# Kernel tuning notes

Measured on AMD Instinct MI355X. Metric: run time of the kernel, lower is better.

## Reference

```python
import jax, jax.numpy as jnp
import numpy as np

N_NODES = 100000


def _gcn_conv(x, W, b, row, col, norm, n):
    # PyG GCNConv: h = x @ W, then symmetric-normalized scatter-add, then bias
    h = x @ W                          # [N, out]
    msg = h[col] * norm[:, None]       # gather at source nodes, scale per-edge
    out = jax.ops.segment_sum(msg, row, num_segments=n)  # scatter-add to dest
    return out + b


def setup_inputs() -> dict:
    key = jax.random.key(0)
    k1, k2, k3, k4, k5, k6 = jax.random.split(key, 6)
    F_in, H, C = 128, 128, 64
    E = 1600000
    x = jax.random.normal(k1, (N_NODES, F_in), dtype=jnp.float32)
    edge_index = jax.random.randint(k2, (2, E), 0, N_NODES, dtype=jnp.int64)
    s1 = 1.0 / np.sqrt(F_in)
    s2 = 1.0 / np.sqrt(H)
    W1 = jax.random.uniform(k3, (F_in, H), jnp.float32, -s1, s1)
    b1 = jax.random.uniform(k4, (H,), jnp.float32, -s1, s1)
    W2 = jax.random.uniform(k5, (H, C), jnp.float32, -s2, s2)
    b2 = jax.random.uniform(k6, (C,), jnp.float32, -s2, s2)
    return {"x": x, "edge_index": edge_index, "W1": W1, "b1": b1, "W2": W2, "b2": b2}


def reference(x, edge_index, W1, b1, W2, b2):
    n = x.shape[0]
    # add self-loops (GCNConv default)
    loops = jnp.arange(n, dtype=edge_index.dtype)
    row = jnp.concatenate([edge_index[0], loops])  # destination
    col = jnp.concatenate([edge_index[1], loops])  # source
    # symmetric normalization deg^{-1/2}[row] * deg^{-1/2}[col]
    deg = jax.ops.segment_sum(jnp.ones_like(row, dtype=x.dtype), row, num_segments=n)
    dinv = jnp.where(deg > 0, jax.lax.rsqrt(deg), 0.0)
    norm = dinv[row] * dinv[col]       # [E+N]
    h = jax.nn.relu(_gcn_conv(x, W1, b1, row, col, norm, n))
    # dropout is identity in eval mode
    out = _gcn_conv(h, W2, b2, row, col, norm, n)
    return jax.nn.log_softmax(out, axis=1)
```

## Files before the change

kernel.cpp:

```cpp
#include <hip/hip_runtime.h>
#include <hip/hip_fp16.h>
#include <cstdint>
#include <cstddef>

#define TPB 256
#define CAP 64
#define FWSHIFT 9
#define FWROWS 512
#define CAPB 96
#define DEC_ITERS 32


using half8 = __attribute__((ext_vector_type(8))) _Float16;
using f32x4 = __attribute__((ext_vector_type(4))) float;

struct GemmSm {
    _Float16 Wl[32 * 64 * 8];
    _Float16 Of[4][16 * 136];
};
struct DecSm { int cur[256]; int bad; };
union SetupSm { GemmSm g; DecSm d; };

__global__ __launch_bounds__(256)
void k_setup(const void* __restrict__ ei, int E, int N,
             const float* __restrict__ W1, const float* __restrict__ W2,
             _Float16* __restrict__ wf2,
             int2* __restrict__ bpairs, int* __restrict__ bcnt,
             int nDec, int nFW,
             const float* __restrict__ x, __half* __restrict__ xw1, int nGemm) {
    __shared__ __align__(16) SetupSm sm;
    const int b = blockIdx.x;
    const int tid = threadIdx.x;

    if (b < 8) {
        int i = b * TPB + tid;
        int k  = i >> 4;
        int n0 = (i & 15) * 4;
        float4 w = ((const float4*)W2)[i];
        int ct = n0 >> 4, kb = k >> 5;
        int lane0 = ((k >> 3) & 3) * 16 + (n0 & 15);
        int j = k & 7;
        int base = ((ct * 4 + kb) * 64 + lane0) * 8 + j;
        wf2[base]      = (_Float16)w.x;
        wf2[base + 8]  = (_Float16)w.y;
        wf2[base + 16] = (_Float16)w.z;
        wf2[base + 24] = (_Float16)w.w;
    } else if (b < 8 + nDec) {
        const int dblk = b - 8;
        if (tid == 0) sm.d.bad = 0;
        for (int f = tid; f < nFW; f += TPB) sm.d.cur[f] = 0;
        __syncthreads();
        {
            long long v = ((const long long*)ei)[tid];
            if (v < 0 || v >= (long long)N) sm.d.bad = 1;
        }
        __syncthreads();
        const int is64 = !sm.d.bad;
        const int base = dblk * (TPB * DEC_ITERS);
        const long long* e64 = (const long long*)ei;
        const int* e32 = (const int*)ei;

        for (int it = 0; it < DEC_ITERS; it += 4) {
            int d[4], s[4]; bool val[4];
#pragma unroll
            for (int k = 0; k < 4; ++k) {
                int e = base + (it + k) * TPB + tid;
                val[k] = e < E;
                if (val[k]) {
                    if (is64) { d[k] = (int)e64[e]; s[k] = (int)e64[(long long)E + e]; }
                    else      { d[k] = e32[e];      s[k] = e32[E + e]; }
                }
            }
#pragma unroll
            for (int k = 0; k < 4; ++k) {
                if (val[k]) {
                    int fw  = d[k] >> FWSHIFT;
                    int pos = atomicAdd(&sm.d.cur[fw], 1);
                    if (pos < CAPB)
                        bpairs[((size_t)fw * nDec + dblk) * CAPB + pos] =
                            make_int2(d[k], s[k]);
                }
            }
        }
        __syncthreads();
        for (int f = tid; f < nFW; f += TPB) {
            int c = sm.d.cur[f];
            bcnt[(size_t)f * nDec + dblk] = c > CAPB ? CAPB : c;
        }
    } else {
        const int gb = b - 8 - nDec;
        for (int i = tid; i < 4096; i += TPB) {
            float4 w = ((const float4*)W1)[i];
            int k  = i >> 5;
            int n0 = (i & 31) * 4;
            int ct = n0 >> 4, kb = k >> 5;
            int lane0 = ((k >> 3) & 3) * 16 + (n0 & 15);
            int j = k & 7;
            int bs = ((ct * 4 + kb) * 64 + lane0) * 8 + j;
            sm.g.Wl[bs]      = (_Float16)w.x;
            sm.g.Wl[bs + 8]  = (_Float16)w.y;
            sm.g.Wl[bs + 16] = (_Float16)w.z;
            sm.g.Wl[bs + 24] = (_Float16)w.w;
        }
        __syncthreads();
        const half8* wl = (const half8*)sm.g.Wl;
        const int wave = tid >> 6, lane = tid & 63;
        const int m = lane & 15, quad = lane >> 4;
        const int nRowTiles = (N + 15) >> 4;

        for (int rt = gb * 4 + wave; rt < nRowTiles; rt += nGemm * 4) {
            const int row0 = rt * 16;
            const int arow = row0 + m;
            const bool rvalid = arow < N;
            const float* xrow = x + (size_t)(rvalid ? arow : 0) * 128;

            f32x4 acc[8];
#pragma unroll
            for (int ct = 0; ct < 8; ++ct) acc[ct] = (f32x4){0.f, 0.f, 0.f, 0.f};

#pragma unroll
            for (int kb = 0; kb < 4; ++kb) {
                const float4* ap = (const float4*)(xrow + kb * 32 + quad * 8);
                float4 a0 = ap[0], a1 = ap[1];
                half8 a;
                a[0] = (_Float16)a0.x; a[1] = (_Float16)a0.y;
                a[2] = (_Float16)a0.z; a[3] = (_Float16)a0.w;
                a[4] = (_Float16)a1.x; a[5] = (_Float16)a1.y;
                a[6] = (_Float16)a1.z; a[7] = (_Float16)a1.w;
#pragma unroll
                for (int ct = 0; ct < 8; ++ct) {
                    half8 bfr = wl[(ct * 4 + kb) * 64 + lane];
                    acc[ct] = __builtin_amdgcn_mfma_f32_16x16x32_f16(a, bfr, acc[ct], 0, 0, 0);
                }
            }

            _Float16* myO = &sm.g.Of[wave][0];
#pragma unroll
            for (int ct = 0; ct < 8; ++ct)
#pragma unroll
                for (int r = 0; r < 4; ++r)
                    myO[(quad * 4 + r) * 136 + ct * 16 + m] = (_Float16)acc[ct][r];
            int vr = N - row0; if (vr > 16) vr = 16;
            float4* dst = (float4*)(xw1 + (size_t)row0 * 128);
            for (int i = lane; i < vr * 16; i += 64) {
                int r = i >> 4, q = i & 15;
                dst[r * 16 + q] = *(const float4*)&myO[r * 136 + q * 8];
            }
        }
    }
}

__global__ __launch_bounds__(256)
void k_fill(const int2* __restrict__ bpairs, const int* __restrict__ bcnt,
            int nDec, int N,
            int* __restrict__ cnt, float* __restrict__ dinv,
            int* __restrict__ slots) {
    __shared__ int cur[FWROWS];
    const int fw = blockIdx.x;
    const int tid = threadIdx.x;
    const int lo = fw << FWSHIFT;
    for (int i = tid; i < FWROWS; i += TPB) cur[i] = 0;
    __syncthreads();

    for (int s = tid; s < nDec; s += TPB) {
        const int c = bcnt[(size_t)fw * nDec + s];
        const int2* bp = bpairs + ((size_t)fw * nDec + s) * CAPB;
        int j = 0;
        for (; j + 3 < c; j += 4) {
            const int4* q4 = (const int4*)(bp + j);
            int4 u0 = q4[0], u1 = q4[1];
            int2 p0 = make_int2(u0.x, u0.y), p1 = make_int2(u0.z, u0.w);
            int2 p2 = make_int2(u1.x, u1.y), p3 = make_int2(u1.z, u1.w);
            int q0 = atomicAdd(&cur[p0.x - lo], 1);
            int q1 = atomicAdd(&cur[p1.x - lo], 1);
            int q2 = atomicAdd(&cur[p2.x - lo], 1);
            int q3 = atomicAdd(&cur[p3.x - lo], 1);
            if (q0 < CAP) slots[(size_t)p0.x * CAP + q0] = p0.y;
            if (q1 < CAP) slots[(size_t)p1.x * CAP + q1] = p1.y;
            if (q2 < CAP) slots[(size_t)p2.x * CAP + q2] = p2.y;
            if (q3 < CAP) slots[(size_t)p3.x * CAP + q3] = p3.y;
        }
        for (; j < c; ++j) {
            int2 p = bp[j];
            int pos = atomicAdd(&cur[p.x - lo], 1);
            if (pos < CAP) slots[(size_t)p.x * CAP + pos] = p.y;
        }
    }
    __syncthreads();
    for (int i = tid; i < FWROWS; i += TPB) {
        int node = lo + i;
        if (node < N) {
            int cc = cur[i];
            cnt[node]  = cc;
            dinv[node] = rsqrtf((float)cc + 1.0f);
        }
    }
}

__global__ __launch_bounds__(256)
void k_g1g2(const __half* __restrict__ xw1, const int* __restrict__ cnt,
            const float* __restrict__ dinv,
            const int* __restrict__ slots, const float* __restrict__ bias,
            const half8* __restrict__ wf2, __half* __restrict__ xw2, int N) {
    __shared__ __align__(16) _Float16 Ht[16 * 136];
    __shared__ __align__(16) _Float16 Of[16 * 72];
    __shared__ float dv16[16];

    const int row0 = blockIdx.x * 16;
    const int local = threadIdx.x >> 4;
    const int lane16 = threadIdx.x & 15;
    const int node = row0 + local;

    {
        union { __half2 h2[4]; float4 f; } u;
        float dvn = 0.f;
        if (node < N) {
            int cn = cnt[node];
            int len = cn > CAP ? CAP : cn;
            dvn = dinv[node];
            const int* sl = slots + (size_t)node * CAP;
            float acc[8];
            {
                float4 raw = *(const float4*)(xw1 + (size_t)node * 128 + lane16 * 8);
                const __half2* hp = (const __half2*)&raw;
#pragma unroll
                for (int k = 0; k < 4; ++k) {
                    float2 f = __half22float2(hp[k]);
                    acc[2 * k] = dvn * f.x; acc[2 * k + 1] = dvn * f.y;
                }
            }
            int j = 0;
            for (; j + 3 < len; j += 4) {
                int4 cc = *(const int4*)(sl + j);
                float dv0 = dinv[cc.x];
                float dv1 = dinv[cc.y];
                float dv2 = dinv[cc.z];
                float dv3 = dinv[cc.w];
                float4 raw0 = *(const float4*)(xw1 + (size_t)cc.x * 128 + lane16 * 8);
                float4 raw1 = *(const float4*)(xw1 + (size_t)cc.y * 128 + lane16 * 8);
                float4 raw2 = *(const float4*)(xw1 + (size_t)cc.z * 128 + lane16 * 8);
                float4 raw3 = *(const float4*)(xw1 + (size_t)cc.w * 128 + lane16 * 8);
                const __half2* h0 = (const __half2*)&raw0;
                const __half2* h1 = (const __half2*)&raw1;
                const __half2* h2 = (const __half2*)&raw2;
                const __half2* h3 = (const __half2*)&raw3;
#pragma unroll
                for (int k = 0; k < 4; ++k) {
                    float2 f0 = __half22float2(h0[k]);
                    float2 f1 = __half22float2(h1[k]);
                    float2 f2 = __half22float2(h2[k]);
                    float2 f3 = __half22float2(h3[k]);
                    acc[2 * k]     = fmaf(dv0, f0.x, fmaf(dv1, f1.x,
                                     fmaf(dv2, f2.x, fmaf(dv3, f3.x, acc[2 * k]))));
                    acc[2 * k + 1] = fmaf(dv0, f0.y, fmaf(dv1, f1.y,
                                     fmaf(dv2, f2.y, fmaf(dv3, f3.y, acc[2 * k + 1]))));
                }
            }
            for (; j < len; ++j) {
                int c = sl[j];
                float dv = dinv[c];
                float4 raw = *(const float4*)(xw1 + (size_t)c * 128 + lane16 * 8);
                const __half2* hp = (const __half2*)&raw;
#pragma unroll
                for (int k = 0; k < 4; ++k) {
                    float2 f = __half22float2(hp[k]);
                    acc[2 * k]     = fmaf(dv, f.x, acc[2 * k]);
                    acc[2 * k + 1] = fmaf(dv, f.y, acc[2 * k + 1]);
                }
            }
            float4 b01 = ((const float4*)bias)[lane16 * 2];
            float4 b23 = ((const float4*)bias)[lane16 * 2 + 1];
            float v[8];
            v[0] = b01.x + dvn * acc[0]; v[1] = b01.y + dvn * acc[1];
            v[2] = b01.z + dvn * acc[2]; v[3] = b01.w + dvn * acc[3];
            v[4] = b23.x + dvn * acc[4]; v[5] = b23.y + dvn * acc[5];
            v[6] = b23.z + dvn * acc[6]; v[7] = b23.w + dvn * acc[7];
#pragma unroll
            for (int k = 0; k < 4; ++k)
                u.h2[k] = __floats2half2_rn(fmaxf(v[2 * k], 0.f), fmaxf(v[2 * k + 1], 0.f));
        } else {
            u.f = make_float4(0.f, 0.f, 0.f, 0.f);
        }
        if (lane16 == 0) dv16[local] = dvn;
        *(float4*)(Ht + local * 136 + lane16 * 8) = u.f;
    }
    __syncthreads();

    {
        const int wave = threadIdx.x >> 6, lane = threadIdx.x & 63;
        const int m = lane & 15, quad = lane >> 4;
        f32x4 acc = (f32x4){0.f, 0.f, 0.f, 0.f};
#pragma unroll
        for (int kb = 0; kb < 4; ++kb) {
            half8 a = *(const half8*)(Ht + m * 136 + kb * 32 + quad * 8);
            half8 b = wf2[(wave * 4 + kb) * 64 + lane];
            acc = __builtin_amdgcn_mfma_f32_16x16x32_f16(a, b, acc, 0, 0, 0);
        }
#pragma unroll
        for (int r = 0; r < 4; ++r)
            Of[(quad * 4 + r) * 72 + wave * 16 + m] =
                (_Float16)(acc[r] * dv16[quad * 4 + r]);
    }
    __syncthreads();
    {
        int vr = N - row0; if (vr > 16) vr = 16;
        float4* dst = (float4*)(xw2 + (size_t)row0 * 64);
        for (int i = threadIdx.x; i < vr * 8; i += TPB) {
            int r = i >> 3, q = i & 7;
            dst[r * 8 + q] = *(const float4*)&Of[r * 72 + q * 8];
        }
    }
}

__global__ void k_gather2_lsm(const __half* __restrict__ xws, const int* __restrict__ cnt,
                              const float* __restrict__ dinv,
                              const int* __restrict__ slots,
                              const float* __restrict__ bias, float* __restrict__ out, int N) {
    long long t = (long long)blockIdx.x * TPB + threadIdx.x;
    int node = (int)(t >> 3);
    int lane = (int)(t & 7);
    if (node >= N) return;
    int cn = cnt[node];
    int len = cn > CAP ? CAP : cn;
    float dvn = dinv[node];
    const int* sl = slots + (size_t)node * CAP;
    float a[8];
    {
        float4 raw = *(const float4*)(xws + (size_t)node * 64 + lane * 8);
        const __half2* hp = (const __half2*)&raw;
#pragma unroll
        for (int k = 0; k < 4; ++k) {
            float2 f = __half22float2(hp[k]);
            a[2 * k] = f.x; a[2 * k + 1] = f.y;
        }
    }
    int j = 0;
    for (; j + 3 < len; j += 4) {
        int4 cc = *(const int4*)(sl + j);
        float4 r0 = *(const float4*)(xws + (size_t)cc.x * 64 + lane * 8);
        float4 r1 = *(const float4*)(xws + (size_t)cc.y * 64 + lane * 8);
        float4 r2 = *(const float4*)(xws + (size_t)cc.z * 64 + lane * 8);
        float4 r3 = *(const float4*)(xws + (size_t)cc.w * 64 + lane * 8);
        const __half2* h0 = (const __half2*)&r0;
        const __half2* h1 = (const __half2*)&r1;
        const __half2* h2 = (const __half2*)&r2;
        const __half2* h3 = (const __half2*)&r3;
#pragma unroll
        for (int k = 0; k < 4; ++k) {
            float2 f0 = __half22float2(h0[k]);
            float2 f1 = __half22float2(h1[k]);
            float2 f2 = __half22float2(h2[k]);
            float2 f3 = __half22float2(h3[k]);
            a[2 * k]     += (f0.x + f1.x) + (f2.x + f3.x);
            a[2 * k + 1] += (f0.y + f1.y) + (f2.y + f3.y);
        }
    }
    for (; j < len; ++j) {
        int c = sl[j];
        float4 raw = *(const float4*)(xws + (size_t)c * 64 + lane * 8);
        const __half2* hp = (const __half2*)&raw;
#pragma unroll
        for (int k = 0; k < 4; ++k) {
            float2 f = __half22float2(hp[k]);
            a[2 * k] += f.x; a[2 * k + 1] += f.y;
        }
    }
    float4 b01 = ((const float4*)bias)[lane * 2];
    float4 b23 = ((const float4*)bias)[lane * 2 + 1];
    float v[8];
    v[0] = b01.x + dvn * a[0]; v[1] = b01.y + dvn * a[1];
    v[2] = b01.z + dvn * a[2]; v[3] = b01.w + dvn * a[3];
    v[4] = b23.x + dvn * a[4]; v[5] = b23.y + dvn * a[5];
    v[6] = b23.z + dvn * a[6]; v[7] = b23.w + dvn * a[7];

    float m = v[0];
#pragma unroll
    for (int k = 1; k < 8; ++k) m = fmaxf(m, v[k]);
#pragma unroll
    for (int off = 1; off < 8; off <<= 1) m = fmaxf(m, __shfl_xor(m, off));
    float s = 0.f;
#pragma unroll
    for (int k = 0; k < 8; ++k) s += expf(v[k] - m);
#pragma unroll
    for (int off = 1; off < 8; off <<= 1) s += __shfl_xor(s, off);
    float ls = m + logf(s);
    float4 o0 = make_float4(v[0] - ls, v[1] - ls, v[2] - ls, v[3] - ls);
    float4 o1 = make_float4(v[4] - ls, v[5] - ls, v[6] - ls, v[7] - ls);
    ((float4*)(out + (size_t)node * 64))[lane * 2]     = o0;
    ((float4*)(out + (size_t)node * 64))[lane * 2 + 1] = o1;
}

extern "C" void kernel_launch(void* const* d_in, const int* in_sizes, int n_in,
                              void* d_out, int out_size, void* d_ws, size_t ws_size,
                              hipStream_t stream) {
    const float* x  = (const float*)d_in[0];
    const void*  ei = d_in[1];
    const float* W1 = (const float*)d_in[2];
    const float* b1 = (const float*)d_in[3];
    const float* W2 = (const float*)d_in[4];
    const float* b2 = (const float*)d_in[5];
    float* out = (float*)d_out;

    const int N = in_sizes[0] / 128;
    const int E = in_sizes[1] / 2;

    const int nFW  = (N + FWROWS - 1) >> FWSHIFT;
    const int nDec = (E + TPB * DEC_ITERS - 1) / (TPB * DEC_ITERS);
    const int nGemm = 512;

    char* base = (char*)d_ws;
    size_t off = 0;
    auto alloc = [&](size_t bytes) { char* p = base + off; off = (off + bytes + 255) & ~(size_t)255; return p; };
    int*      cnt    = (int*)alloc((size_t)N * sizeof(int));
    float*    dinv   = (float*)alloc((size_t)N * sizeof(float));
    _Float16* wf2    = (_Float16*)alloc(128 * 64 * sizeof(_Float16));
    int*      bcnt   = (int*)alloc((size_t)nFW * nDec * sizeof(int));
    int2*     bpairs = (int2*)alloc((size_t)nFW * nDec * CAPB * sizeof(int2));
    int*      slots  = (int*)alloc((size_t)N * CAP * sizeof(int));
    __half*   xw1    = (__half*)alloc((size_t)N * 128 * sizeof(__half));
    __half*   xw2    = (__half*)alloc((size_t)N * 64 * sizeof(__half));
    (void)ws_size;

    const int nodeTiles = (N + 15) / 16;

    k_setup<<<8 + nDec + nGemm, TPB, 0, stream>>>(ei, E, N, W1, W2, wf2,
                                                  bpairs, bcnt, nDec, nFW,
                                                  x, xw1, nGemm);

    k_fill<<<nFW, TPB, 0, stream>>>(bpairs, bcnt, nDec, N, cnt, dinv, slots);

    k_g1g2<<<nodeTiles, TPB, 0, stream>>>(xw1, cnt, dinv, slots, b1,
                                          (const half8*)wf2, xw2, N);

    {
        long long t = (long long)N * 8;
        k_gather2_lsm<<<(int)((t + TPB - 1) / TPB), TPB, 0, stream>>>(xw2, cnt, dinv, slots, b2, out, N);
    }
}
```

Measured before the change: 244.6 us.

## Pack edge pairs into one int and merge fill with the x@W1 GEMM

Edge bucket entries are packed into a single 32-bit word (9-bit local destination plus 17-bit source) instead of an int2, halving the bucket buffer traffic. The x@W1 GEMM blocks move out of the decode kernel into the fill kernel, so the GEMM runs alongside the slot fill rather than alongside the decode. Slot index loads in the gather kernels use nontemporal loads. The packing assumes node ids fit in 17 bits, which holds for N=100000 but not for larger graphs.

```diff
diff --git a/kernel.cpp b/kernel.cpp
--- a/kernel.cpp
+++ b/kernel.cpp
@@ -13,22 +13,20 @@
 
 using half8 = __attribute__((ext_vector_type(8))) _Float16;
 using f32x4 = __attribute__((ext_vector_type(4))) float;
+using i32x4 = __attribute__((ext_vector_type(4))) int;
 
 struct GemmSm {
     _Float16 Wl[32 * 64 * 8];
     _Float16 Of[4][16 * 136];
 };
-struct DecSm { int cur[256]; int bad; };
-union SetupSm { GemmSm g; DecSm d; };
+struct FillSm { int cur[FWROWS]; };
+union MegaSm { GemmSm g; FillSm f; };
 
 __global__ __launch_bounds__(256)
 void k_setup(const void* __restrict__ ei, int E, int N,
-             const float* __restrict__ W1, const float* __restrict__ W2,
-             _Float16* __restrict__ wf2,
-             int2* __restrict__ bpairs, int* __restrict__ bcnt,
-             int nDec, int nFW,
-             const float* __restrict__ x, __half* __restrict__ xw1, int nGemm) {
-    __shared__ __align__(16) SetupSm sm;
+             const float* __restrict__ W2, _Float16* __restrict__ wf2,
+             int* __restrict__ bpack, int* __restrict__ bcnt,
+             int nDec, int nFW) {
     const int b = blockIdx.x;
     const int tid = threadIdx.x;
 
@@ -45,17 +43,19 @@
         wf2[base + 8]  = (_Float16)w.y;
         wf2[base + 16] = (_Float16)w.z;
         wf2[base + 24] = (_Float16)w.w;
-    } else if (b < 8 + nDec) {
+    } else {
+        __shared__ int cur[256];
+        __shared__ int bad;
         const int dblk = b - 8;
-        if (tid == 0) sm.d.bad = 0;
-        for (int f = tid; f < nFW; f += TPB) sm.d.cur[f] = 0;
+        if (tid == 0) bad = 0;
+        for (int f = tid; f < nFW; f += TPB) cur[f] = 0;
         __syncthreads();
         {
             long long v = ((const long long*)ei)[tid];
-            if (v < 0 || v >= (long long)N) sm.d.bad = 1;
-        }
-        __syncthreads();
-        const int is64 = !sm.d.bad;
+            if (v < 0 || v >= (long long)N) bad = 1;
+        }
+        __syncthreads();
+        const int is64 = !bad;
         const int base = dblk * (TPB * DEC_ITERS);
         const long long* e64 = (const long long*)ei;
         const int* e32 = (const int*)ei;
@@ -75,20 +75,74 @@
             for (int k = 0; k < 4; ++k) {
                 if (val[k]) {
                     int fw  = d[k] >> FWSHIFT;
-                    int pos = atomicAdd(&sm.d.cur[fw], 1);
+                    int pos = atomicAdd(&cur[fw], 1);
                     if (pos < CAPB)
-                        bpairs[((size_t)fw * nDec + dblk) * CAPB + pos] =
-                            make_int2(d[k], s[k]);
+                        bpack[((size_t)fw * nDec + dblk) * CAPB + pos] =
+                            ((d[k] & (FWROWS - 1)) << 17) | s[k];
                 }
             }
         }
         __syncthreads();
         for (int f = tid; f < nFW; f += TPB) {
-            int c = sm.d.cur[f];
+            int c = cur[f];
             bcnt[(size_t)f * nDec + dblk] = c > CAPB ? CAPB : c;
         }
+    }
+}
+
+__global__ __launch_bounds__(256)
+void k_mega(const int* __restrict__ bpack, const int* __restrict__ bcnt,
+            int nDec, int N,
+            int* __restrict__ cnt, float* __restrict__ dinv,
+            int* __restrict__ slots,
+            const float* __restrict__ x, const float* __restrict__ W1,
+            __half* __restrict__ xw1, int nFW, int nGemm) {
+    __shared__ __align__(16) MegaSm sm;
+    const int tid = threadIdx.x;
+
+    if ((int)blockIdx.x < nFW) {
+        const int fw = blockIdx.x;
+        const int lo = fw << FWSHIFT;
+        for (int i = tid; i < FWROWS; i += TPB) sm.f.cur[i] = 0;
+        __syncthreads();
+
+        for (int s = tid; s < nDec; s += TPB) {
+            const int c = bcnt[(size_t)fw * nDec + s];
+            const int* bp = bpack + ((size_t)fw * nDec + s) * CAPB;
+            int j = 0;
+            for (; j + 3 < c; j += 4) {
+                i32x4 u = __builtin_nontemporal_load((const i32x4*)(bp + j));
+                int dl0 = u[0] >> 17, s0 = u[0] & 0x1FFFF;
+                int dl1 = u[1] >> 17, s1 = u[1] & 0x1FFFF;
+                int dl2 = u[2] >> 17, s2 = u[2] & 0x1FFFF;
+                int dl3 = u[3] >> 17, s3 = u[3] & 0x1FFFF;
+                int q0 = atomicAdd(&sm.f.cur[dl0], 1);
+                int q1 = atomicAdd(&sm.f.cur[dl1], 1);
+                int q2 = atomicAdd(&sm.f.cur[dl2], 1);
+                int q3 = atomicAdd(&sm.f.cur[dl3], 1);
+                if (q0 < CAP) slots[(size_t)(lo + dl0) * CAP + q0] = s0;
+                if (q1 < CAP) slots[(size_t)(lo + dl1) * CAP + q1] = s1;
+                if (q2 < CAP) slots[(size_t)(lo + dl2) * CAP + q2] = s2;
+                if (q3 < CAP) slots[(size_t)(lo + dl3) * CAP + q3] = s3;
+            }
+            for (; j < c; ++j) {
+                int v = __builtin_nontemporal_load(bp + j);
+                int dl = v >> 17, sv = v & 0x1FFFF;
+                int pos = atomicAdd(&sm.f.cur[dl], 1);
+                if (pos < CAP) slots[(size_t)(lo + dl) * CAP + pos] = sv;
+            }
+        }
+        __syncthreads();
+        for (int i = tid; i < FWROWS; i += TPB) {
+            int node = lo + i;
+            if (node < N) {
+                int cc = sm.f.cur[i];
+                cnt[node]  = cc;
+                dinv[node] = rsqrtf((float)cc + 1.0f);
+            }
+        }
     } else {
-        const int gb = b - 8 - nDec;
+        const int gb = (int)blockIdx.x - nFW;
         for (int i = tid; i < 4096; i += TPB) {
             float4 w = ((const float4*)W1)[i];
             int k  = i >> 5;
@@ -151,53 +205,6 @@
 }
 
 __global__ __launch_bounds__(256)
-void k_fill(const int2* __restrict__ bpairs, const int* __restrict__ bcnt,
-            int nDec, int N,
-            int* __restrict__ cnt, float* __restrict__ dinv,
-            int* __restrict__ slots) {
-    __shared__ int cur[FWROWS];
-    const int fw = blockIdx.x;
-    const int tid = threadIdx.x;
-    const int lo = fw << FWSHIFT;
-    for (int i = tid; i < FWROWS; i += TPB) cur[i] = 0;
-    __syncthreads();
-
-    for (int s = tid; s < nDec; s += TPB) {
-        const int c = bcnt[(size_t)fw * nDec + s];
-        const int2* bp = bpairs + ((size_t)fw * nDec + s) * CAPB;
-        int j = 0;
-        for (; j + 3 < c; j += 4) {
-            const int4* q4 = (const int4*)(bp + j);
-            int4 u0 = q4[0], u1 = q4[1];
-            int2 p0 = make_int2(u0.x, u0.y), p1 = make_int2(u0.z, u0.w);
-            int2 p2 = make_int2(u1.x, u1.y), p3 = make_int2(u1.z, u1.w);
-            int q0 = atomicAdd(&cur[p0.x - lo], 1);
-            int q1 = atomicAdd(&cur[p1.x - lo], 1);
-            int q2 = atomicAdd(&cur[p2.x - lo], 1);
-            int q3 = atomicAdd(&cur[p3.x - lo], 1);
-            if (q0 < CAP) slots[(size_t)p0.x * CAP + q0] = p0.y;
-            if (q1 < CAP) slots[(size_t)p1.x * CAP + q1] = p1.y;
-            if (q2 < CAP) slots[(size_t)p2.x * CAP + q2] = p2.y;
-            if (q3 < CAP) slots[(size_t)p3.x * CAP + q3] = p3.y;
-        }
-        for (; j < c; ++j) {
-            int2 p = bp[j];
-            int pos = atomicAdd(&cur[p.x - lo], 1);
-            if (pos < CAP) slots[(size_t)p.x * CAP + pos] = p.y;
-        }
-    }
-    __syncthreads();
-    for (int i = tid; i < FWROWS; i += TPB) {
-        int node = lo + i;
-        if (node < N) {
-            int cc = cur[i];
-            cnt[node]  = cc;
-            dinv[node] = rsqrtf((float)cc + 1.0f);
-        }
-    }
-}
-
-__global__ __launch_bounds__(256)
 void k_g1g2(const __half* __restrict__ xw1, const int* __restrict__ cnt,
             const float* __restrict__ dinv,
             const int* __restrict__ slots, const float* __restrict__ bias,
@@ -231,15 +238,15 @@
             }
             int j = 0;
             for (; j + 3 < len; j += 4) {
-                int4 cc = *(const int4*)(sl + j);
-                float dv0 = dinv[cc.x];
-                float dv1 = dinv[cc.y];
-                float dv2 = dinv[cc.z];
-                float dv3 = dinv[cc.w];
-                float4 raw0 = *(const float4*)(xw1 + (size_t)cc.x * 128 + lane16 * 8);
-                float4 raw1 = *(const float4*)(xw1 + (size_t)cc.y * 128 + lane16 * 8);
-                float4 raw2 = *(const float4*)(xw1 + (size_t)cc.z * 128 + lane16 * 8);
-                float4 raw3 = *(const float4*)(xw1 + (size_t)cc.w * 128 + lane16 * 8);
+                i32x4 cc = __builtin_nontemporal_load((const i32x4*)(sl + j));
+                float dv0 = dinv[cc[0]];
+                float dv1 = dinv[cc[1]];
+                float dv2 = dinv[cc[2]];
+                float dv3 = dinv[cc[3]];
+                float4 raw0 = *(const float4*)(xw1 + (size_t)cc[0] * 128 + lane16 * 8);
+                float4 raw1 = *(const float4*)(xw1 + (size_t)cc[1] * 128 + lane16 * 8);
+                float4 raw2 = *(const float4*)(xw1 + (size_t)cc[2] * 128 + lane16 * 8);
+                float4 raw3 = *(const float4*)(xw1 + (size_t)cc[3] * 128 + lane16 * 8);
                 const __half2* h0 = (const __half2*)&raw0;
                 const __half2* h1 = (const __half2*)&raw1;
                 const __half2* h2 = (const __half2*)&raw2;
@@ -257,7 +264,7 @@
                 }
             }
             for (; j < len; ++j) {
-                int c = sl[j];
+                int c = __builtin_nontemporal_load(sl + j);
                 float dv = dinv[c];
                 float4 raw = *(const float4*)(xw1 + (size_t)c * 128 + lane16 * 8);
                 const __half2* hp = (const __half2*)&raw;
@@ -336,11 +343,11 @@
     }
     int j = 0;
     for (; j + 3 < len; j += 4) {
-        int4 cc = *(const int4*)(sl + j);
-        float4 r0 = *(const float4*)(xws + (size_t)cc.x * 64 + lane * 8);
-        float4 r1 = *(const float4*)(xws + (size_t)cc.y * 64 + lane * 8);
-        float4 r2 = *(const float4*)(xws + (size_t)cc.z * 64 + lane * 8);
-        float4 r3 = *(const float4*)(xws + (size_t)cc.w * 64 + lane * 8);
+        i32x4 cc = __builtin_nontemporal_load((const i32x4*)(sl + j));
+        float4 r0 = *(const float4*)(xws + (size_t)cc[0] * 64 + lane * 8);
+        float4 r1 = *(const float4*)(xws + (size_t)cc[1] * 64 + lane * 8);
+        float4 r2 = *(const float4*)(xws + (size_t)cc[2] * 64 + lane * 8);
+        float4 r3 = *(const float4*)(xws + (size_t)cc[3] * 64 + lane * 8);
         const __half2* h0 = (const __half2*)&r0;
         const __half2* h1 = (const __half2*)&r1;
         const __half2* h2 = (const __half2*)&r2;
@@ -356,7 +363,7 @@
         }
     }
     for (; j < len; ++j) {
-        int c = sl[j];
+        int c = __builtin_nontemporal_load(sl + j);
         float4 raw = *(const float4*)(xws + (size_t)c * 64 + lane * 8);
         const __half2* hp = (const __half2*)&raw;
 #pragma unroll
@@ -415,7 +422,7 @@
     float*    dinv   = (float*)alloc((size_t)N * sizeof(float));
     _Float16* wf2    = (_Float16*)alloc(128 * 64 * sizeof(_Float16));
     int*      bcnt   = (int*)alloc((size_t)nFW * nDec * sizeof(int));
-    int2*     bpairs = (int2*)alloc((size_t)nFW * nDec * CAPB * sizeof(int2));
+    int*      bpack  = (int*)alloc((size_t)nFW * nDec * CAPB * sizeof(int));
     int*      slots  = (int*)alloc((size_t)N * CAP * sizeof(int));
     __half*   xw1    = (__half*)alloc((size_t)N * 128 * sizeof(__half));
     __half*   xw2    = (__half*)alloc((size_t)N * 64 * sizeof(__half));
@@ -423,11 +430,11 @@
 
     const int nodeTiles = (N + 15) / 16;
 
-    k_setup<<<8 + nDec + nGemm, TPB, 0, stream>>>(ei, E, N, W1, W2, wf2,
-                                                  bpairs, bcnt, nDec, nFW,
-                                                  x, xw1, nGemm);
-
-    k_fill<<<nFW, TPB, 0, stream>>>(bpairs, bcnt, nDec, N, cnt, dinv, slots);
+    k_setup<<<8 + nDec, TPB, 0, stream>>>(ei, E, N, W2, wf2, bpack, bcnt,
+                                          nDec, nFW);
+
+    k_mega<<<nFW + nGemm, TPB, 0, stream>>>(bpack, bcnt, nDec, N, cnt, dinv,
+                                            slots, x, W1, xw1, nFW, nGemm);
 
     k_g1g2<<<nodeTiles, TPB, 0, stream>>>(xw1, cnt, dinv, slots, b1,
                                           (const half8*)wf2, xw2, N);
```

After: 260.1 us. +6.3%, slower.
